# Kernel optimization log

Measured on AMD Instinct MI355X. Metric: run time of the kernel, lower is better.

## Reference

```python
import jax, jax.numpy as jnp
import numpy as np

K_CURV = 1.0   # manifold curvature k
KERNEL = 5
STRIDE = 1
PAD = 2


def setup_inputs() -> dict:
    key = jax.random.key(0)
    k1, k2, k3 = jax.random.split(key, 3)
    bsz, L, Cin, Cout = 16, 8192, 64, 64
    # Build points on the Lorentz manifold: time = sqrt(||space||^2 + k)
    space = jax.random.normal(k1, (bsz, L, Cin - 1), dtype=jnp.float32)
    time = jnp.sqrt(jnp.sum(space ** 2, axis=-1, keepdims=True) + K_CURV)
    x = jnp.concatenate([time, space], axis=-1)  # (bs, len, Cin)
    lin_feat = (Cin - 1) * KERNEL + 1            # 316
    W = jax.random.normal(k2, (Cout, lin_feat), dtype=jnp.float32) / np.sqrt(lin_feat).astype(np.float32)
    b = jax.random.normal(k3, (Cout,), dtype=jnp.float32) * 0.01
    return {"x": x, "W": W, "b": b}


def reference(x, W, b):
    bsz, L, C = x.shape
    sqrt_k = jnp.sqrt(jnp.asarray(K_CURV, x.dtype))
    # pad along length, then clamp time component to sqrt(k) (F.pad + clamp_)
    xp = jnp.pad(x, ((0, 0), (PAD, PAD), (0, 0)))
    xp = xp.at[..., 0].set(jnp.maximum(xp[..., 0], sqrt_k))
    L_out = (L + 2 * PAD - KERNEL) // STRIDE + 1
    # unfold(1, K, stride): gather overlapping windows -> (bs, L_out, K, C)
    idx = jnp.arange(L_out)[:, None] * STRIDE + jnp.arange(KERNEL)[None, :]
    patches = xp[:, idx, :]
    patches = jnp.swapaxes(patches, 2, 3)        # (bs, L_out, C, K) as torch unfold
    # Lorentz time rescale over the K time coords of each patch
    p_time = patches[:, :, 0, :]                 # (bs, L_out, K)
    t_resc = jnp.sqrt(jnp.sum(p_time ** 2, axis=-1, keepdims=True)
                      - (KERNEL - 1) * K_CURV)   # (bs, L_out, 1)
    p_space = patches[:, :, 1:, :].reshape(bsz, L_out, -1)  # (bs, L_out, (C-1)*K)
    feats = jnp.concatenate([t_resc, p_space], axis=-1)     # (bs, L_out, lin_feat)
    # LorentzFullyConnected: linear, then recompute time from space norm
    y = jnp.einsum('blf,of->blo', feats, W) + b              # (bs, L_out, Cout)
    y_space = y[..., 1:]
    y_time = jnp.sqrt(jnp.sum(y_space ** 2, axis=-1, keepdims=True) + K_CURV)
    return jnp.concatenate([y_time, y_space], axis=-1)
```

## Files before the change

### kernel.cpp

```cpp
#include <hip/hip_runtime.h>
#include <math.h>


#define BSZ   16
#define LLEN  8192
#define CIN   64
#define COUT  64
#define KW    5
#define LINF  316
#define MTILE 64
#define ROWS  68
#define ASTR  72
#define KB    320
#define TPB   2
#define NTILES (BSZ * LLEN / MTILE)
#define GRID   (NTILES / TPB)

typedef __attribute__((ext_vector_type(8))) short  short8;
typedef __attribute__((ext_vector_type(4))) float  float4v;

__device__ inline unsigned short f2bf(float f) {
    unsigned u = __builtin_bit_cast(unsigned int, f);
    u += 0x7FFFu + ((u >> 16) & 1u);
    return (unsigned short)(u >> 16);
}

template <int CTRL>
__device__ inline float dpp_add(float v) {
    int x = __builtin_bit_cast(int, v);
    int t = __builtin_amdgcn_update_dpp(0, x, CTRL, 0xF, 0xF, true);
    return v + __builtin_bit_cast(float, t);
}

__device__ inline float dpp_rowsum16_hi(float v) {
    v = dpp_add<0x111>(v);
    v = dpp_add<0x112>(v);
    v = dpp_add<0x114>(v);
    v = dpp_add<0x118>(v);
    return v;
}

__global__ __launch_bounds__(256) void prep_W(const float* __restrict__ W,
                                              unsigned short* __restrict__ Wb) {
    int i = blockIdx.x * 256 + threadIdx.x;
    if (i >= COUT * KB) return;
    int n   = i / KB;
    int kk  = i - n * KB;
    int tap = kk >> 6;
    int c   = kk & 63;
    float v = (c == 0) ? 0.f : W[n * LINF + 1 + (c - 1) * KW + tap];
    Wb[i] = f2bf(v);
}

__global__ __launch_bounds__(256, 4) void lorentz_mfma(
    const float* __restrict__ x, const unsigned short* __restrict__ Wb,
    const float* __restrict__ W, const float* __restrict__ bias,
    float* __restrict__ out)
{
    __shared__ unsigned short At[2][ROWS * ASTR];
    __shared__ float tcol[2][72];
    __shared__ float pss[2][4][64];

    int tid  = threadIdx.x;
    int lane = tid & 63;
    int nq   = tid >> 6;
    int col  = lane & 15, quad = lane >> 4;
    int n    = nq * 16 + col;

    int tile0 = blockIdx.x * TPB;

    float4 sreg[5];
    bool   sin[5];

    auto stage_load = [&](int tile) {
        int b  = tile >> 7;
        int l0 = (tile & 127) * MTILE;
        const float* xb = x + ((size_t)b * LLEN) * CIN;
        #pragma unroll
        for (int itc = 0; itc < 5; ++itc) {
            int i = tid + itc * 256;
            if (i < ROWS * 16) {
                int r = i >> 4, ch = i & 15;
                int row = l0 - 2 + r;
                sin[itc] = (row >= 0) && (row < LLEN);
                int rowc = min(max(row, 0), LLEN - 1);
                sreg[itc] = ((const float4*)(xb + (size_t)rowc * CIN))[ch];
            }
        }
    };
    auto stage_write = [&](int nb) {
        #pragma unroll
        for (int itc = 0; itc < 5; ++itc) {
            int i = tid + itc * 256;
            if (i < ROWS * 16) {
                int r = i >> 4, ch = i & 15;
                float4 v = sreg[itc];
                if (!sin[itc]) { v.x = (ch == 0) ? 1.f : 0.f; v.y = 0.f; v.z = 0.f; v.w = 0.f; }
                if (ch == 0) tcol[nb][r] = v.x;
                ushort4 pk;
                pk.x = f2bf(v.x); pk.y = f2bf(v.y); pk.z = f2bf(v.z); pk.w = f2bf(v.w);
                *(ushort4*)&At[nb][r * ASTR + ch * 4] = pk;
            }
        }
    };

    stage_load(tile0);

    short8 breg[10];
    {
        const unsigned short* bp = Wb + (size_t)n * KB + quad * 8;
        #pragma unroll
        for (int kk = 0; kk < 10; ++kk)
            breg[kk] = *(const short8*)(bp + kk * 32);
    }
    float bo = bias[n];
    float w0 = W[(size_t)n * LINF];

    stage_write(0);
    __syncthreads();

    int cur = 0;
    #pragma unroll
    for (int it = 0; it < TPB; ++it) {
        int tile = tile0 + it;
        bool more = (it + 1 < TPB);
        if (more) stage_load(tile + 1);

        float4v acc[4];
        #pragma unroll
        for (int ms = 0; ms < 4; ++ms) acc[ms] = (float4v){0.f, 0.f, 0.f, 0.f};
        #pragma unroll
        for (int kk = 0; kk < 10; ++kk) {
            int tap = kk >> 1, ks = kk & 1;
            #pragma unroll
            for (int ms = 0; ms < 4; ++ms) {
                short8 afr = *(const short8*)&At[cur][(ms * 16 + col + tap) * ASTR
                                                     + ks * 32 + quad * 8];
                acc[ms] = __builtin_amdgcn_mfma_f32_16x16x32_bf16(afr, breg[kk], acc[ms], 0, 0, 0);
            }
        }

        #pragma unroll
        for (int ms = 0; ms < 4; ++ms) {
            int p0 = ms * 16 + quad * 4;
            float4 a = *(const float4*)&tcol[cur][p0];
            float4 c = *(const float4*)&tcol[cur][p0 + 4];
            float tw[8] = {a.x, a.y, a.z, a.w, c.x, c.y, c.z, c.w};
            float sq[4];
            #pragma unroll
            for (int reg = 0; reg < 4; ++reg) {
                float s = 0.f;
                #pragma unroll
                for (int t = 0; t < KW; ++t) { float v = tw[reg + t]; s += v * v; }
                float trs = sqrtf(s - (float)(KW - 1));
                float v = acc[ms][reg] + bo + trs * w0;
                acc[ms][reg] = v;
                bool isc0 = (nq == 0) && (col == 0);
                sq[reg] = isc0 ? 0.f : v * v;
            }
            #pragma unroll
            for (int reg = 0; reg < 4; ++reg) {
                float rs = dpp_rowsum16_hi(sq[reg]);
                if (col == 15)
                    pss[cur][nq][ms * 16 + quad * 4 + reg] = rs;
            }
        }

        if (more) stage_write(cur ^ 1);
        __syncthreads();

        #pragma unroll
        for (int ms = 0; ms < 4; ++ms) {
            #pragma unroll
            for (int reg = 0; reg < 4; ++reg) {
                int row = ms * 16 + quad * 4 + reg;
                float v = acc[ms][reg];
                if (nq == 0 && col == 0) {
                    float tot = pss[cur][0][row] + pss[cur][1][row]
                              + pss[cur][2][row] + pss[cur][3][row];
                    v = sqrtf(tot + 1.f);
                }
                out[((size_t)tile * MTILE + row) * COUT + n] = v;
            }
        }
        cur ^= 1;
    }
}

extern "C" void kernel_launch(void* const* d_in, const int* in_sizes, int n_in,
                              void* d_out, int out_size, void* d_ws, size_t ws_size,
                              hipStream_t stream) {
    const float* x    = (const float*)d_in[0];
    const float* W    = (const float*)d_in[1];
    const float* bias = (const float*)d_in[2];
    float* out = (float*)d_out;
    unsigned short* Wb = (unsigned short*)d_ws;

    hipLaunchKernelGGL(prep_W, dim3((COUT * KB + 255) / 256), dim3(256), 0, stream,
                       W, Wb);
    hipLaunchKernelGGL(lorentz_mfma, dim3(GRID), dim3(256), 0, stream,
                       x, Wb, W, bias, out);
}
```

Before: 98.03 us.

## Fuse weight bf16 conversion into main kernel via shared-memory staging

Removes the separate prep_W launch. Each block now reads the fp32 weight matrix, converts it to bf16 and scatters it into shared memory, which aliases the A-tile buffer, then loads its B fragments from there. This saves one kernel launch and the global round trip for the converted weights. In exchange, every one of the 1024 blocks redoes the 20K-element weight conversion, with strided scattered LDS writes and extra barriers. The shared-memory footprint grows to 40KB, which may limit occupancy.

```diff
diff --git a/kernel.cpp b/kernel.cpp
--- a/kernel.cpp
+++ b/kernel.cpp
@@ -16,6 +16,10 @@
 #define NTILES (BSZ * LLEN / MTILE)
 #define GRID   (NTILES / TPB)
 
+#define SMEM_BYTES 40960
+#define TCOL_OFF   19584
+#define PSS_OFF    20160
+
 typedef __attribute__((ext_vector_type(8))) short  short8;
 typedef __attribute__((ext_vector_type(4))) float  float4v;
 
@@ -40,32 +44,21 @@
     return v;
 }
 
-__global__ __launch_bounds__(256) void prep_W(const float* __restrict__ W,
-                                              unsigned short* __restrict__ Wb) {
-    int i = blockIdx.x * 256 + threadIdx.x;
-    if (i >= COUT * KB) return;
-    int n   = i / KB;
-    int kk  = i - n * KB;
-    int tap = kk >> 6;
-    int c   = kk & 63;
-    float v = (c == 0) ? 0.f : W[n * LINF + 1 + (c - 1) * KW + tap];
-    Wb[i] = f2bf(v);
-}
-
 __global__ __launch_bounds__(256, 4) void lorentz_mfma(
-    const float* __restrict__ x, const unsigned short* __restrict__ Wb,
-    const float* __restrict__ W, const float* __restrict__ bias,
-    float* __restrict__ out)
+    const float* __restrict__ x, const float* __restrict__ W,
+    const float* __restrict__ bias, float* __restrict__ out)
 {
-    __shared__ unsigned short At[2][ROWS * ASTR];
-    __shared__ float tcol[2][72];
-    __shared__ float pss[2][4][64];
+    __shared__ __attribute__((aligned(16))) char smem[SMEM_BYTES];
+    unsigned short* WbL  = (unsigned short*)smem;
+    unsigned short* AtB  = (unsigned short*)smem;
+    float*          tcolB = (float*)(smem + TCOL_OFF);
+    float*          pssB  = (float*)(smem + PSS_OFF);
 
     int tid  = threadIdx.x;
     int lane = tid & 63;
     int nq   = tid >> 6;
     int col  = lane & 15, quad = lane >> 4;
-    int n    = nq * 16 + col;
+    int nch  = nq * 16 + col;
 
     int tile0 = blockIdx.x * TPB;
 
@@ -89,6 +82,8 @@
         }
     };
     auto stage_write = [&](int nb) {
+        unsigned short* At = AtB + nb * (ROWS * ASTR);
+        float* tc = tcolB + nb * 72;
         #pragma unroll
         for (int itc = 0; itc < 5; ++itc) {
             int i = tid + itc * 256;
@@ -96,25 +91,41 @@
                 int r = i >> 4, ch = i & 15;
                 float4 v = sreg[itc];
                 if (!sin[itc]) { v.x = (ch == 0) ? 1.f : 0.f; v.y = 0.f; v.z = 0.f; v.w = 0.f; }
-                if (ch == 0) tcol[nb][r] = v.x;
+                if (ch == 0) tc[r] = v.x;
                 ushort4 pk;
                 pk.x = f2bf(v.x); pk.y = f2bf(v.y); pk.z = f2bf(v.z); pk.w = f2bf(v.w);
-                *(ushort4*)&At[nb][r * ASTR + ch * 4] = pk;
+                *(ushort4*)&At[r * ASTR + ch * 4] = pk;
             }
         }
     };
 
     stage_load(tile0);
+
+    #pragma unroll
+    for (int i = tid; i < COUT * KW; i += 256) {
+        int n = i / KW, tap = i - n * KW;
+        WbL[n * KB + tap * 64] = 0;
+    }
+    for (int i = tid; i < COUT * LINF; i += 256) {
+        float v = W[i];
+        int n = i / LINF, f = i - n * LINF;
+        if (f > 0) {
+            int c1 = (f - 1) / KW, tap = (f - 1) - c1 * KW;
+            WbL[n * KB + tap * 64 + c1 + 1] = f2bf(v);
+        }
+    }
+    __syncthreads();
 
     short8 breg[10];
     {
-        const unsigned short* bp = Wb + (size_t)n * KB + quad * 8;
+        const unsigned short* bp = WbL + (size_t)nch * KB + quad * 8;
         #pragma unroll
         for (int kk = 0; kk < 10; ++kk)
             breg[kk] = *(const short8*)(bp + kk * 32);
     }
-    float bo = bias[n];
-    float w0 = W[(size_t)n * LINF];
+    float bo = bias[nch];
+    float w0 = W[(size_t)nch * LINF];
+    __syncthreads();
 
     stage_write(0);
     __syncthreads();
@@ -126,6 +137,10 @@
         bool more = (it + 1 < TPB);
         if (more) stage_load(tile + 1);
 
+        const unsigned short* At = AtB + cur * (ROWS * ASTR);
+        const float* tc = tcolB + cur * 72;
+        float* pss = pssB + cur * 4 * 64;
+
         float4v acc[4];
         #pragma unroll
         for (int ms = 0; ms < 4; ++ms) acc[ms] = (float4v){0.f, 0.f, 0.f, 0.f};
@@ -134,8 +149,8 @@
             int tap = kk >> 1, ks = kk & 1;
             #pragma unroll
             for (int ms = 0; ms < 4; ++ms) {
-                short8 afr = *(const short8*)&At[cur][(ms * 16 + col + tap) * ASTR
-                                                     + ks * 32 + quad * 8];
+                short8 afr = *(const short8*)&At[(ms * 16 + col + tap) * ASTR
+                                                 + ks * 32 + quad * 8];
                 acc[ms] = __builtin_amdgcn_mfma_f32_16x16x32_bf16(afr, breg[kk], acc[ms], 0, 0, 0);
             }
         }
@@ -143,8 +158,8 @@
         #pragma unroll
         for (int ms = 0; ms < 4; ++ms) {
             int p0 = ms * 16 + quad * 4;
-            float4 a = *(const float4*)&tcol[cur][p0];
-            float4 c = *(const float4*)&tcol[cur][p0 + 4];
+            float4 a = *(const float4*)&tc[p0];
+            float4 c = *(const float4*)&tc[p0 + 4];
             float tw[8] = {a.x, a.y, a.z, a.w, c.x, c.y, c.z, c.w};
             float sq[4];
             #pragma unroll
@@ -162,7 +177,7 @@
             for (int reg = 0; reg < 4; ++reg) {
                 float rs = dpp_rowsum16_hi(sq[reg]);
                 if (col == 15)
-                    pss[cur][nq][ms * 16 + quad * 4 + reg] = rs;
+                    pss[nq * 64 + ms * 16 + quad * 4 + reg] = rs;
             }
         }
 
@@ -176,11 +191,11 @@
                 int row = ms * 16 + quad * 4 + reg;
                 float v = acc[ms][reg];
                 if (nq == 0 && col == 0) {
-                    float tot = pss[cur][0][row] + pss[cur][1][row]
-                              + pss[cur][2][row] + pss[cur][3][row];
+                    float tot = pss[0 * 64 + row] + pss[1 * 64 + row]
+                              + pss[2 * 64 + row] + pss[3 * 64 + row];
                     v = sqrtf(tot + 1.f);
                 }
-                out[((size_t)tile * MTILE + row) * COUT + n] = v;
+                out[((size_t)tile * MTILE + row) * COUT + nch] = v;
             }
         }
         cur ^= 1;
@@ -194,10 +209,8 @@
     const float* W    = (const float*)d_in[1];
     const float* bias = (const float*)d_in[2];
     float* out = (float*)d_out;
-    unsigned short* Wb = (unsigned short*)d_ws;
-
-    hipLaunchKernelGGL(prep_W, dim3((COUT * KB + 255) / 256), dim3(256), 0, stream,
-                       W, Wb);
+    (void)d_ws; (void)ws_size;
+
     hipLaunchKernelGGL(lorentz_mfma, dim3(GRID), dim3(256), 0, stream,
-                       x, Wb, W, bias, out);
-}
+                       x, W, bias, out);
+}
```

Measured after the change: 118.6 us. 21.0% more time.
